# Performance work log

Hardware: AMD Instinct MI355X
Metric: run time of the kernel (lower is better)

Reference implementation:

```python
import jax, jax.numpy as jnp
import numpy as np

EMBED_DIM = 1024
N_HEADS = 16
HEAD_DIM = EMBED_DIM // N_HEADS


def setup_inputs() -> dict:
    key = jax.random.key(0)
    ks = jax.random.split(key, 9)
    s = 1.0 / np.sqrt(EMBED_DIM)
    x = jax.random.normal(ks[0], (4, 2048, EMBED_DIM), dtype=jnp.float32)
    Wq = jax.random.uniform(ks[1], (EMBED_DIM, EMBED_DIM), jnp.float32, -s, s)
    bq = jax.random.uniform(ks[2], (EMBED_DIM,), jnp.float32, -s, s)
    Wk = jax.random.uniform(ks[3], (EMBED_DIM, EMBED_DIM), jnp.float32, -s, s)
    bk = jax.random.uniform(ks[4], (EMBED_DIM,), jnp.float32, -s, s)
    Wv = jax.random.uniform(ks[5], (EMBED_DIM, EMBED_DIM), jnp.float32, -s, s)
    bv = jax.random.uniform(ks[6], (EMBED_DIM,), jnp.float32, -s, s)
    Wo = jax.random.uniform(ks[7], (EMBED_DIM, EMBED_DIM), jnp.float32, -s, s)
    bo = jax.random.uniform(ks[8], (EMBED_DIM,), jnp.float32, -s, s)
    return {"x": x, "Wq": Wq, "bq": bq, "Wk": Wk, "bk": bk,
            "Wv": Wv, "bv": bv, "Wo": Wo, "bo": bo}


def reference(x, Wq, bq, Wk, bk, Wv, bv, Wo, bo):
    B, S, _ = x.shape
    # projections (PyTorch Linear: x @ W.T + b; weights stored as [in,out] here)
    q = x @ Wq + bq
    k = x @ Wk + bk
    v = x @ Wv + bv
    # [B, H, S, D]
    q = q.reshape(B, S, N_HEADS, HEAD_DIM).transpose(0, 2, 1, 3)
    k = k.reshape(B, S, N_HEADS, HEAD_DIM).transpose(0, 2, 1, 3)
    v = v.reshape(B, S, N_HEADS, HEAD_DIM).transpose(0, 2, 1, 3)
    scores = jnp.einsum('bhsd,bhtd->bhst', q, k) / np.sqrt(HEAD_DIM).astype(np.float32)
    attn = jax.nn.softmax(scores, axis=-1)
    out = jnp.einsum('bhst,bhtd->bhsd', attn, v)
    out = out.transpose(0, 2, 1, 3).reshape(B, S, EMBED_DIM)
    return out @ Wo + bo  # dropout=0 (eval) -> identity
```

## Files before the change

kernel.cpp:

```cpp
#include <hip/hip_runtime.h>
#include <stdint.h>

#define EMBED 1024
#define NH 16
#define HD 64
#define SEQ 2048
#define BATCH 4
#define M_TOT (BATCH*SEQ)
#define QSCALE 0.18033688011112042f

typedef __attribute__((ext_vector_type(8))) short short8;
typedef __attribute__((ext_vector_type(4))) float floatx4;
typedef __attribute__((ext_vector_type(4))) unsigned int uintx4;

__device__ __forceinline__ unsigned short f2bf(float f) {
    union { float f; unsigned int u; } v; v.f = f;
    unsigned int r = v.u + 0x7fffu + ((v.u >> 16) & 1u);
    return (unsigned short)(r >> 16);
}

__device__ __forceinline__ void load_lds16(const unsigned short* g, unsigned short* l) {
    __builtin_amdgcn_global_load_lds(
        (const __attribute__((address_space(1))) unsigned int*)g,
        (__attribute__((address_space(3))) unsigned int*)l, 16, 0, 0);
}

__global__ void cvt_x(const float* __restrict__ x, unsigned short* __restrict__ xb) {
    int i = (blockIdx.x * 256 + threadIdx.x) * 4;
    float4 v = *(const float4*)(x + i);
    ushort4 o;
    o.x = f2bf(v.x); o.y = f2bf(v.y); o.z = f2bf(v.z); o.w = f2bf(v.w);
    *(ushort4*)(xb + i) = o;
}

__global__ void wtrans(const float* __restrict__ w0, const float* __restrict__ w1,
                       const float* __restrict__ w2, const float* __restrict__ w3,
                       unsigned short* __restrict__ t0, unsigned short* __restrict__ t1,
                       unsigned short* __restrict__ t2, unsigned short* __restrict__ t3) {
    __shared__ float tile[32][33];
    const float* W; unsigned short* T;
    switch (blockIdx.z) { case 0: W=w0; T=t0; break; case 1: W=w1; T=t1; break;
                          case 2: W=w2; T=t2; break; default: W=w3; T=t3; }
    int n0 = blockIdx.x * 32, k0 = blockIdx.y * 32;
    int tx = threadIdx.x, ty = threadIdx.y;
    #pragma unroll
    for (int i = 0; i < 4; i++)
        tile[ty + i*8][tx] = W[(k0 + ty + i*8) * EMBED + n0 + tx];
    __syncthreads();
    #pragma unroll
    for (int i = 0; i < 4; i++)
        T[(n0 + ty + i*8) * EMBED + k0 + tx] = f2bf(tile[tx][ty + i*8]);
}

template<int MODE>
__global__ __launch_bounds__(512, 4) void gemmk(
        const unsigned short* __restrict__ A, const unsigned short* __restrict__ BT,
        const float* __restrict__ b0, const float* __restrict__ b1, const float* __restrict__ b2,
        void* __restrict__ o0, void* __restrict__ o1, void* __restrict__ o2) {
    constexpr int BM = 128, BN = 128;
    constexpr int BUFS = (BM+BN)*32;
    __shared__ unsigned short lds[128*136];
    const int tid = threadIdx.x;
    const int lane = tid & 63, wave = tid >> 6;
    const int quad = lane >> 4, l16 = lane & 15;
    const int wm = wave >> 2, wn = wave & 3;
    const int id = blockIdx.x;
    constexpr int MS = (M_TOT/BM)/8;
    const int xcd = id & 7, j = id >> 3;
    const int mblk = (xcd * MS + (j % MS)) * BM;
    const int nblk = (j / MS) * BN;

    const int srow = tid >> 2;
    const int scol = ((tid & 3) ^ (srow & 3)) * 8;
    const unsigned short* Asrc = A  + (size_t)(mblk + srow) * EMBED + scol;
    const unsigned short* Bsrc = BT + (size_t)(nblk + srow) * EMBED + scol;
    unsigned short* sda = lds + wave * 512;
    unsigned short* sdb = lds + BM*32 + wave * 512;

    const int cs = (quad ^ (l16 & 3)) * 8;
    const unsigned short* Abase = lds + (wm*64 + l16)*32 + cs;
    const unsigned short* Bbase = lds + BM*32 + (wn*32 + l16)*32 + cs;

    floatx4 acc[4][2];
    #pragma unroll
    for (int m=0;m<4;m++)
      #pragma unroll
      for (int n=0;n<2;n++) acc[m][n] = (floatx4){0.f,0.f,0.f,0.f};

#define ST(t_) do { \
    const int buf_ = (t_) & 1; const int ko_ = (t_)*32; \
    load_lds16(Asrc + ko_, sda + buf_*BUFS); \
    load_lds16(Bsrc + ko_, sdb + buf_*BUFS); \
  } while(0)

    ST(0);
    asm volatile("s_waitcnt vmcnt(0)" ::: "memory");
    asm volatile("s_barrier" ::: "memory");

    #pragma unroll 2
    for (int t = 0; t < 32; ++t) {
        const int bo = (t & 1) * BUFS;
        short8 fA[4], fB[2];
        #pragma unroll
        for (int m=0;m<4;m++) fA[m] = *(const short8*)(Abase + bo + m*512);
        #pragma unroll
        for (int n=0;n<2;n++) fB[n] = *(const short8*)(Bbase + bo + n*512);
        if (t < 31) ST(t+1);
        #pragma unroll
        for (int m=0;m<4;m++)
          #pragma unroll
          for (int n=0;n<2;n++)
            acc[m][n] = __builtin_amdgcn_mfma_f32_16x16x32_bf16(fA[m], fB[n], acc[m][n], 0,0,0);
        if (t < 31) {
            asm volatile("s_waitcnt vmcnt(0)" ::: "memory");
            asm volatile("s_barrier" ::: "memory");
        }
    }
#undef ST

    if constexpr (MODE == 1) {
        float* O = (float*)o0;
        #pragma unroll
        for (int mt=0;mt<4;mt++)
          #pragma unroll
          for (int nt=0;nt<2;nt++) {
            int col = nblk + wn*32 + nt*16 + l16;
            float bv = b0[col];
            #pragma unroll
            for (int r=0;r<4;r++) {
                int row = mblk + wm*64 + mt*16 + quad*4 + r;
                O[(size_t)row * EMBED + col] = acc[mt][nt][r] + bv;
            }
          }
    } else {
        int which = nblk >> 10;
        const float* bs = (which==0) ? b0 : (which==1) ? b1 : b2;
        if (which < 2) {
            unsigned short* O = (unsigned short*)((which==0) ? o0 : o1);
            float sc = (which==0) ? QSCALE : 1.f;
            #pragma unroll
            for (int mt=0;mt<4;mt++)
              #pragma unroll
              for (int nt=0;nt<2;nt++) {
                int coll = (nblk & 1023) + wn*32 + nt*16 + l16;
                float bv = bs[coll];
                int h = coll >> 6, d = coll & 63;
                #pragma unroll
                for (int r=0;r<4;r++) {
                    int row = mblk + wm*64 + mt*16 + quad*4 + r;
                    int b = row >> 11, s = row & 2047;
                    O[((size_t)(b*NH + h)*SEQ + s)*HD + d] = f2bf((acc[mt][nt][r] + bv) * sc);
                }
              }
        } else {
            unsigned short* T = lds;
            unsigned short* OV = (unsigned short*)o2;
            size_t rowbase = ((size_t)((mblk >> 11)*1024 + (nblk & 1023))) * SEQ + (mblk & 2047);
            __syncthreads();
            #pragma unroll
            for (int nt=0;nt<2;nt++) {
                int cloc = wn*32 + nt*16 + l16;
                float bv = bs[(nblk & 1023) + cloc];
                #pragma unroll
                for (int mt=0;mt<4;mt++) {
                    int row0 = wm*64 + mt*16 + quad*4;
                    int sp0 = (row0 & ~31) | (((row0 >> 2) & 3) << 3) | (((row0 >> 4) & 1) << 2);
                    ushort4 w;
                    w.x = f2bf(acc[mt][nt][0] + bv);
                    w.y = f2bf(acc[mt][nt][1] + bv);
                    w.z = f2bf(acc[mt][nt][2] + bv);
                    w.w = f2bf(acc[mt][nt][3] + bv);
                    *(ushort4*)(T + cloc*136 + sp0) = w;
                }
            }
            __syncthreads();
            int s0 = (lane & 15) * 8, dloc = lane >> 4;
            #pragma unroll
            for (int i=0;i<4;i++) {
                int c = wave*16 + i*4 + dloc;
                short8 v = *(const short8*)(T + c*136 + s0);
                *(short8*)(OV + rowbase + (size_t)c * SEQ + s0) = v;
            }
        }
    }
}

__global__ __launch_bounds__(512, 4) void attn(
    const unsigned short* __restrict__ Q, const unsigned short* __restrict__ K,
    const unsigned short* __restrict__ VTp, unsigned short* __restrict__ O) {
    __shared__ unsigned short kv[2][4096];
    unsigned short* kvf = &kv[0][0];
    int tid = threadIdx.x;
    int lane = tid & 63, wave = tid >> 6;
    int quad = lane >> 4, l16 = lane & 15;
    int id = blockIdx.x;
    int bh = (id & 7) * 8 + (id >> 6);
    int qblk = (id >> 3) & 7;
    int b = bh >> 4, h = bh & 15;
    int q0 = qblk * 256 + wave * 32;
    const unsigned short* Qb = Q + (size_t)bh * SEQ * HD;
    const unsigned short* Kb = K + (size_t)bh * SEQ * HD;
    const unsigned short* Vb = VTp + (size_t)bh * HD * SEQ;
    int li = (wave & 3) * 64 + lane;
    const unsigned short* src;
    int dstofs = (wave & 3) * 512 + ((wave >> 2) ? 2048 : 0);
    int src_step;
    if (wave < 4) {
        int t = li >> 3, slot = li & 7;
        int dblk = slot ^ (t & 7);
        src = Kb + (size_t)t * HD + dblk * 8;
        src_step = 32 * HD;
    } else {
        int d = li >> 2, slot = li & 3;
        int swz = (d & 3) ^ ((d >> 2) & 3);
        src = Vb + (size_t)d * SEQ + (slot ^ swz) * 8;
        src_step = 32;
    }
    short8 qf[2][2];
    #pragma unroll
    for (int mt=0;mt<2;mt++) {
        const unsigned short* qp = Qb + (size_t)(q0 + mt*16 + l16) * HD + quad*8;
        qf[mt][0] = *(const short8*)(qp);
        qf[mt][1] = *(const short8*)(qp + 32);
    }
    floatx4 o_acc[2][4], l_acc[2];
    #pragma unroll
    for (int mt=0;mt<2;mt++) {
        l_acc[mt] = (floatx4){0.f,0.f,0.f,0.f};
        #pragma unroll
        for (int dt=0;dt<4;dt++) o_acc[mt][dt] = (floatx4){0.f,0.f,0.f,0.f};
    }
    short8 ones;
    #pragma unroll
    for (int jj=0;jj<8;jj++) ones[jj] = (short)0x3F80;
    int koff[2][2], voff[4];
    #pragma unroll
    for (int nt=0;nt<2;nt++) {
        int t = nt*16 + l16;
        #pragma unroll
        for (int hh=0;hh<2;hh++)
            koff[nt][hh] = t*64 + ((hh*4 + quad) ^ (t & 7)) * 8;
    }
    #pragma unroll
    for (int dt=0;dt<4;dt++) {
        int d = dt*16 + l16;
        voff[dt] = 2048 + d*32 + ((quad ^ (d & 3) ^ ((d >> 2) & 3))) * 8;
    }

    load_lds16(src, kvf + dstofs);
    src += src_step;

    for (int it = 0; it < 64; ++it) {
        const unsigned short* kb = kvf + (it & 1) * 4096;
        if (it < 63) {
            load_lds16(src, kvf + ((it & 1) ^ 1) * 4096 + dstofs);
            src += src_step;
            asm volatile("s_waitcnt vmcnt(1)" ::: "memory");
        } else {
            asm volatile("s_waitcnt vmcnt(0)" ::: "memory");
        }
        __builtin_amdgcn_s_barrier();
        asm volatile("" ::: "memory");
        short8 kf[2][2], vf[4];
        #pragma unroll
        for (int nt=0;nt<2;nt++) {
            kf[nt][0] = *(const short8*)(kb + koff[nt][0]);
            kf[nt][1] = *(const short8*)(kb + koff[nt][1]);
        }
        #pragma unroll
        for (int dt=0;dt<4;dt++)
            vf[dt] = *(const short8*)(kb + voff[dt]);
        floatx4 sacc[2][2];
        __builtin_amdgcn_s_setprio(1);
        #pragma unroll
        for (int nt=0;nt<2;nt++)
          #pragma unroll
          for (int mt=0;mt<2;mt++) {
            floatx4 s = (floatx4){0.f,0.f,0.f,0.f};
            s = __builtin_amdgcn_mfma_f32_16x16x32_bf16(kf[nt][0], qf[mt][0], s, 0, 0, 0);
            s = __builtin_amdgcn_mfma_f32_16x16x32_bf16(kf[nt][1], qf[mt][1], s, 0, 0, 0);
            sacc[nt][mt] = s;
          }
        __builtin_amdgcn_s_setprio(0);
        short8 pf[2];
        #pragma unroll
        for (int mt=0;mt<2;mt++) {
            uintx4 pu;
            #pragma unroll
            for (int jp=0;jp<4;jp++) {
                int nt = jp >> 1, rp = (jp & 1) * 2;
                float e0 = __builtin_amdgcn_exp2f(sacc[nt][mt][rp]);
                float e1 = __builtin_amdgcn_exp2f(sacc[nt][mt][rp+1]);
                unsigned int w;
                asm("v_cvt_pk_bf16_f32 %0, %1, %2" : "=v"(w) : "v"(e0), "v"(e1));
                pu[jp] = w;
            }
            pf[mt] = __builtin_bit_cast(short8, pu);
        }
        __builtin_amdgcn_s_setprio(1);
        #pragma unroll
        for (int mt=0;mt<2;mt++) {
            l_acc[mt] = __builtin_amdgcn_mfma_f32_16x16x32_bf16(ones, pf[mt], l_acc[mt], 0, 0, 0);
            #pragma unroll
            for (int dt=0;dt<4;dt++)
                o_acc[mt][dt] = __builtin_amdgcn_mfma_f32_16x16x32_bf16(vf[dt], pf[mt], o_acc[mt][dt], 0, 0, 0);
        }
        __builtin_amdgcn_s_setprio(0);
        asm volatile("" ::: "memory");
        __builtin_amdgcn_s_barrier();
    }
    #pragma unroll
    for (int mt=0;mt<2;mt++) {
        float inv = 1.f / l_acc[mt][0];
        int s = q0 + mt*16 + l16;
        #pragma unroll
        for (int dt=0;dt<4;dt++) {
            ushort4 w;
            w.x = f2bf(o_acc[mt][dt][0]*inv);
            w.y = f2bf(o_acc[mt][dt][1]*inv);
            w.z = f2bf(o_acc[mt][dt][2]*inv);
            w.w = f2bf(o_acc[mt][dt][3]*inv);
            *(ushort4*)(O + ((size_t)b*SEQ + s)*EMBED + h*HD + dt*16 + quad*4) = w;
        }
    }
}

extern "C" void kernel_launch(void* const* d_in, const int* in_sizes, int n_in,
                              void* d_out, int out_size, void* d_ws, size_t ws_size,
                              hipStream_t stream) {
    const float* x  = (const float*)d_in[0];
    const float* Wq = (const float*)d_in[1]; const float* bq = (const float*)d_in[2];
    const float* Wk = (const float*)d_in[3]; const float* bk = (const float*)d_in[4];
    const float* Wv = (const float*)d_in[5]; const float* bv = (const float*)d_in[6];
    const float* Wo = (const float*)d_in[7]; const float* bo = (const float*)d_in[8];
    char* ws = (char*)d_ws;
    unsigned short* xb  = (unsigned short*)(ws);
    unsigned short* WqT = (unsigned short*)(ws + (16ull<<20));
    unsigned short* WkT = (unsigned short*)(ws + (18ull<<20));
    unsigned short* WvT = (unsigned short*)(ws + (20ull<<20));
    unsigned short* WoT = (unsigned short*)(ws + (22ull<<20));
    unsigned short* Qb  = (unsigned short*)(ws + (24ull<<20));
    unsigned short* Kb  = (unsigned short*)(ws + (40ull<<20));
    unsigned short* VTb = (unsigned short*)(ws + (56ull<<20));
    unsigned short* Ob  = xb;

    cvt_x<<<(M_TOT*EMBED)/1024, 256, 0, stream>>>(x, xb);
    wtrans<<<dim3(32,32,4), dim3(32,8), 0, stream>>>(Wq,Wk,Wv,Wo, WqT,WkT,WvT,WoT);
    gemmk<0><<<dim3(1536), 512, 0, stream>>>(xb, WqT, bq, bk, bv, Qb, Kb, VTb);
    attn<<<dim3(512), 512, 0, stream>>>(Qb, Kb, VTb, Ob);
    gemmk<1><<<dim3(512), 512, 0, stream>>>(Ob, WoT, bo, bo, bo, (float*)d_out, nullptr, nullptr);
}
```

Baseline: 260.4 us.

## Deepen GEMM LDS pipeline to four stages and widen LDS swizzle

```diff
diff --git a/kernel.cpp b/kernel.cpp
--- a/kernel.cpp
+++ b/kernel.cpp
@@ -52,14 +52,41 @@
         T[(n0 + ty + i*8) * EMBED + k0 + tx] = f2bf(tile[tx][ty + i*8]);
 }
 
+#define GBUFS 8192
+
+template<bool STG, int WAITN>
+__device__ __forceinline__ void ktile(int t,
+        const unsigned short* Abase, const unsigned short* Bbase,
+        const unsigned short* Asrc, const unsigned short* Bsrc,
+        unsigned short* sda, unsigned short* sdb, floatx4 (&acc)[4][2]) {
+    const int bo = (t & 3) * GBUFS;
+    short8 fA[4], fB[2];
+    #pragma unroll
+    for (int m=0;m<4;m++) fA[m] = *(const short8*)(Abase + bo + m*512);
+    #pragma unroll
+    for (int n=0;n<2;n++) fB[n] = *(const short8*)(Bbase + bo + n*512);
+    if (STG) {
+        const int buf_ = (t+3) & 3; const int ko_ = (t+3)*32;
+        load_lds16(Asrc + ko_, sda + buf_*GBUFS);
+        load_lds16(Bsrc + ko_, sdb + buf_*GBUFS);
+    }
+    #pragma unroll
+    for (int m=0;m<4;m++)
+      #pragma unroll
+      for (int n=0;n<2;n++)
+        acc[m][n] = __builtin_amdgcn_mfma_f32_16x16x32_bf16(fA[m], fB[n], acc[m][n], 0,0,0);
+    if (WAITN == 4)      { asm volatile("s_waitcnt vmcnt(4)" ::: "memory"); asm volatile("s_barrier" ::: "memory"); }
+    else if (WAITN == 2) { asm volatile("s_waitcnt vmcnt(2)" ::: "memory"); asm volatile("s_barrier" ::: "memory"); }
+    else if (WAITN == 0) { asm volatile("s_waitcnt vmcnt(0)" ::: "memory"); asm volatile("s_barrier" ::: "memory"); }
+}
+
 template<int MODE>
 __global__ __launch_bounds__(512, 4) void gemmk(
         const unsigned short* __restrict__ A, const unsigned short* __restrict__ BT,
         const float* __restrict__ b0, const float* __restrict__ b1, const float* __restrict__ b2,
         void* __restrict__ o0, void* __restrict__ o1, void* __restrict__ o2) {
     constexpr int BM = 128, BN = 128;
-    constexpr int BUFS = (BM+BN)*32;
-    __shared__ unsigned short lds[128*136];
+    __shared__ unsigned short lds[4*GBUFS];
     const int tid = threadIdx.x;
     const int lane = tid & 63, wave = tid >> 6;
     const int quad = lane >> 4, l16 = lane & 15;
@@ -71,13 +98,13 @@
     const int nblk = (j / MS) * BN;
 
     const int srow = tid >> 2;
-    const int scol = ((tid & 3) ^ (srow & 3)) * 8;
+    const int scol = ((tid & 3) ^ (srow & 3) ^ ((srow >> 2) & 3)) * 8;
     const unsigned short* Asrc = A  + (size_t)(mblk + srow) * EMBED + scol;
     const unsigned short* Bsrc = BT + (size_t)(nblk + srow) * EMBED + scol;
     unsigned short* sda = lds + wave * 512;
     unsigned short* sdb = lds + BM*32 + wave * 512;
 
-    const int cs = (quad ^ (l16 & 3)) * 8;
+    const int cs = (quad ^ (l16 & 3) ^ ((l16 >> 2) & 3)) * 8;
     const unsigned short* Abase = lds + (wm*64 + l16)*32 + cs;
     const unsigned short* Bbase = lds + BM*32 + (wn*32 + l16)*32 + cs;
 
@@ -87,36 +114,21 @@
       #pragma unroll
       for (int n=0;n<2;n++) acc[m][n] = (floatx4){0.f,0.f,0.f,0.f};
 
-#define ST(t_) do { \
-    const int buf_ = (t_) & 1; const int ko_ = (t_)*32; \
-    load_lds16(Asrc + ko_, sda + buf_*BUFS); \
-    load_lds16(Bsrc + ko_, sdb + buf_*BUFS); \
-  } while(0)
-
-    ST(0);
-    asm volatile("s_waitcnt vmcnt(0)" ::: "memory");
+    #pragma unroll
+    for (int p=0;p<3;p++) {
+        load_lds16(Asrc + p*32, sda + p*GBUFS);
+        load_lds16(Bsrc + p*32, sdb + p*GBUFS);
+    }
+    asm volatile("s_waitcnt vmcnt(4)" ::: "memory");
     asm volatile("s_barrier" ::: "memory");
 
-    #pragma unroll 2
-    for (int t = 0; t < 32; ++t) {
-        const int bo = (t & 1) * BUFS;
-        short8 fA[4], fB[2];
-        #pragma unroll
-        for (int m=0;m<4;m++) fA[m] = *(const short8*)(Abase + bo + m*512);
-        #pragma unroll
-        for (int n=0;n<2;n++) fB[n] = *(const short8*)(Bbase + bo + n*512);
-        if (t < 31) ST(t+1);
-        #pragma unroll
-        for (int m=0;m<4;m++)
-          #pragma unroll
-          for (int n=0;n<2;n++)
-            acc[m][n] = __builtin_amdgcn_mfma_f32_16x16x32_bf16(fA[m], fB[n], acc[m][n], 0,0,0);
-        if (t < 31) {
-            asm volatile("s_waitcnt vmcnt(0)" ::: "memory");
-            asm volatile("s_barrier" ::: "memory");
-        }
-    }
-#undef ST
+    #pragma unroll 4
+    for (int t = 0; t < 28; ++t)
+        ktile<true,4>(t, Abase, Bbase, Asrc, Bsrc, sda, sdb, acc);
+    ktile<true, 4>(28, Abase, Bbase, Asrc, Bsrc, sda, sdb, acc);
+    ktile<false,2>(29, Abase, Bbase, Asrc, Bsrc, sda, sdb, acc);
+    ktile<false,0>(30, Abase, Bbase, Asrc, Bsrc, sda, sdb, acc);
+    ktile<false,-1>(31, Abase, Bbase, Asrc, Bsrc, sda, sdb, acc);
 
     if constexpr (MODE == 1) {
         float* O = (float*)o0;
```

After: 248.6 us. 4.5% less time.
